# Kernel tuning notes

Hardware: AMD Instinct MI355X
Metric: run time of the kernel (lower is better)

The kernel has to match this reference:

```python
import jax, jax.numpy as jnp
import numpy as np

K = 1024          # num_embeddings
D = 128           # embedding_dim
EMA_DECAY = 0.99
EPS = 1e-5


def setup_inputs() -> dict:
    key = jax.random.key(0)
    k1, k2, k3 = jax.random.split(key, 3)
    z = jax.random.normal(k1, (64, D, 32, 32), dtype=jnp.float32)
    codebook = jax.random.normal(k2, (K, D), dtype=jnp.float32)
    ema_count = jnp.zeros((K,), dtype=jnp.float32)
    ema_weight = jax.random.normal(k3, (K, D), dtype=jnp.float32)
    return {"z": z, "codebook": codebook, "ema_count": ema_count, "ema_weight": ema_weight}


def reference(z, codebook, ema_count, ema_weight):
    B, C, H, W = z.shape
    # flatten to [N, D] in BHWC order (matches permute(0,2,3,1).view(-1, D))
    z_flat = jnp.transpose(z, (0, 2, 3, 1)).reshape(-1, D)  # [N, D]

    # squared euclidean distances [N, K]
    distances = (
        jnp.sum(z_flat * z_flat, axis=1, keepdims=True)
        + jnp.sum(codebook * codebook, axis=1)
        - 2.0 * jnp.matmul(z_flat, codebook.T)
    )
    indices = jnp.argmin(distances, axis=1)  # [N] int

    # gather instead of one-hot @ codebook (same math)
    quantized_flat = codebook[indices]  # [N, D]
    # NOTE: faithful to original: raw view of BHWC-ordered flat buffer into z.shape
    quantized = quantized_flat.reshape(z.shape)

    # EMA statistics (no_grad in original): segment sums instead of one-hot matmuls
    encodings_sum = jax.ops.segment_sum(jnp.ones_like(indices, dtype=jnp.float32), indices, num_segments=K)
    dw = jax.ops.segment_sum(z_flat, indices, num_segments=K)  # [K, D]
    new_ema_count = EMA_DECAY * ema_count + (1.0 - EMA_DECAY) * encodings_sum
    new_ema_weight = EMA_DECAY * ema_weight + (1.0 - EMA_DECAY) * dw
    n = jnp.sum(new_ema_count)
    weights = (new_ema_count + EPS) / (n + K * EPS) * n
    new_codebook = new_ema_weight / weights[:, None]

    commitment_loss = jnp.mean((jax.lax.stop_gradient(quantized) - z) ** 2)
    codebook_loss = jnp.mean((quantized - jax.lax.stop_gradient(z)) ** 2)

    # straight-through estimator
    quantized_st = z + jax.lax.stop_gradient(quantized - z)

    idx_map = indices.reshape(B, H, W)
    return (quantized_st, idx_map, commitment_loss, codebook_loss,
            new_codebook, new_ema_count, new_ema_weight)
```

## Files before the change

### kernel.cpp

```cpp
#include <hip/hip_runtime.h>

#define NVEC 65536
#define KCB  1024
#define DIM  128
#define HW   1024
#define CHUNK 64
#define NCHUNKS (NVEC / CHUNK)

typedef __bf16 b16;
typedef b16 b16x8 __attribute__((ext_vector_type(8)));
typedef float f32x16 __attribute__((ext_vector_type(16)));

static __device__ __forceinline__ unsigned short f2bf(float f) {
  unsigned int x = __float_as_uint(f);
  unsigned int r = x + 0x7fffu + ((x >> 16) & 1u);
  return (unsigned short)(r >> 16);
}

__global__ void k_prep(const float* __restrict__ cb, const float* __restrict__ emw,
                       uint4* __restrict__ cbt, float* __restrict__ ccb,
                       double* __restrict__ cc64, float* __restrict__ out6,
                       int* __restrict__ hist) {
  const int t = blockIdx.x * blockDim.x + threadIdx.x;
  const int kc = t >> 11, u = t & 2047;
  const int code7 = u & 127, dch = u >> 7;
  const float* src = cb + (kc * 128 + code7) * 128 + dch * 8;
  const float4 x = *(const float4*)src;
  const float4 y = *(const float4*)(src + 4);
  uint4 o;
  o.x = (unsigned)f2bf(x.x) | ((unsigned)f2bf(x.y) << 16);
  o.y = (unsigned)f2bf(x.z) | ((unsigned)f2bf(x.w) << 16);
  o.z = (unsigned)f2bf(y.x) | ((unsigned)f2bf(y.y) << 16);
  o.w = (unsigned)f2bf(y.z) | ((unsigned)f2bf(y.w) << 16);
  cbt[t] = o;
  const float4 e0 = *(const float4*)(emw + (size_t)t * 8);
  const float4 e1 = *(const float4*)(emw + (size_t)t * 8 + 4);
  *(float2*)(out6 + (size_t)t * 8 + 0) = make_float2(0.99f * e0.x, 0.99f * e0.y);
  *(float2*)(out6 + (size_t)t * 8 + 2) = make_float2(0.99f * e0.z, 0.99f * e0.w);
  *(float2*)(out6 + (size_t)t * 8 + 4) = make_float2(0.99f * e1.x, 0.99f * e1.y);
  *(float2*)(out6 + (size_t)t * 8 + 6) = make_float2(0.99f * e1.z, 0.99f * e1.w);
  if (t < KCB) hist[t] = 0;
  if (blockIdx.x < 4) {
    const int k = blockIdx.x * 256 + threadIdx.x;
    const float* row = cb + k * DIM;
    double s = 0.0;
#pragma unroll 8
    for (int j = 0; j < DIM; ++j) {
      const double v = (double)row[j];
      s = fma(v, v, s);
    }
    cc64[k] = s;
    ccb[k] = 512.f - 0.5f * (float)s;
  }
}

__global__ __launch_bounds__(256, 4) void k_argmin6(
    const float* __restrict__ z, const uint4* __restrict__ cbt,
    const float* __restrict__ ccb, const double* __restrict__ cc64,
    const float* __restrict__ cb, float* __restrict__ z_t,
    float* __restrict__ out1, int* __restrict__ hist) {
  __shared__ __align__(16) float zs[128][65];
  __shared__ uint2 cand[64][2];
  uint4* Bs = (uint4*)zs;
  const int tid = threadIdx.x;
  const int l = tid & 63, wv = tid >> 6;
  const int g = l >> 5;
  const int lm = l & 31;
  const int wr = (wv & 1) * 32;
  const int wc = wv >> 1;
  const int n0 = blockIdx.x * 64;
  const int b = n0 >> 10;
  const int hwbase = n0 & (HW - 1);

  {
    const int hw4 = (tid & 15) * 4;
    const int dr = tid >> 4;
    const float* src = z + (size_t)b * 131072 + hwbase + hw4;
#pragma unroll
    for (int j = 0; j < 8; ++j) {
      const int d = dr + 16 * j;
      const float4 v = *(const float4*)(src + d * 1024);
      zs[d][hw4 + 0] = v.x; zs[d][hw4 + 1] = v.y;
      zs[d][hw4 + 2] = v.z; zs[d][hw4 + 3] = v.w;
    }
  }
  __syncthreads();

#pragma unroll
  for (int jj = 0; jj < 2; ++jj) {
    const int row = (tid >> 3) + 32 * jj;
    float* dst = z_t + ((size_t)(n0 + row)) * 128;
#pragma unroll
    for (int j = 0; j < 4; ++j) {
      const int d = (j * 8 + (tid & 7)) * 4;
      float4 v;
      v.x = zs[d + 0][row]; v.y = zs[d + 1][row];
      v.z = zs[d + 2][row]; v.w = zs[d + 3][row];
      *(float4*)(dst + d) = v;
    }
  }
  uint4 afrag[8];
  {
    const int row = wr + lm;
#pragma unroll
    for (int ks = 0; ks < 8; ++ks) {
      const int d0 = ks * 16 + g * 8;
      afrag[ks].x = (unsigned)f2bf(zs[d0 + 0][row]) | ((unsigned)f2bf(zs[d0 + 1][row]) << 16);
      afrag[ks].y = (unsigned)f2bf(zs[d0 + 2][row]) | ((unsigned)f2bf(zs[d0 + 3][row]) << 16);
      afrag[ks].z = (unsigned)f2bf(zs[d0 + 4][row]) | ((unsigned)f2bf(zs[d0 + 5][row]) << 16);
      afrag[ks].w = (unsigned)f2bf(zs[d0 + 6][row]) | ((unsigned)f2bf(zs[d0 + 7][row]) << 16);
    }
  }

  unsigned pm1[16], pm2[16];
#pragma unroll
  for (int r = 0; r < 16; ++r) { pm1[r] = 0u; pm2[r] = 0u; }

  for (int kc = 0; kc < 8; ++kc) {
    __syncthreads();
#pragma unroll
    for (int i = 0; i < 8; ++i) {
      __builtin_amdgcn_global_load_lds(&cbt[kc * 2048 + wv * 512 + i * 64 + l],
                                       &Bs[wv * 512 + i * 64], 16, 0, 0);
    }
    const float cv0 = ccb[kc * 128 + (wc * 2 + 0) * 32 + lm];
    const float cv1 = ccb[kc * 128 + (wc * 2 + 1) * 32 + lm];
    __syncthreads();

    f32x16 a0, a1;
#pragma unroll
    for (int j = 0; j < 16; ++j) { a0[j] = cv0; a1[j] = cv1; }
#pragma unroll
    for (int ks = 0; ks < 8; ++ks) {
      const b16x8 av = *reinterpret_cast<const b16x8*>(&afrag[ks]);
      const b16x8 bv0 = *reinterpret_cast<const b16x8*>(&Bs[(ks * 2 + g) * 128 + (wc * 2) * 32 + lm]);
      const b16x8 bv1 = *reinterpret_cast<const b16x8*>(&Bs[(ks * 2 + g) * 128 + (wc * 2 + 1) * 32 + lm]);
      a0 = __builtin_amdgcn_mfma_f32_32x32x16_bf16(av, bv0, a0, 0, 0, 0);
      a1 = __builtin_amdgcn_mfma_f32_32x32x16_bf16(av, bv1, a1, 0, 0, 0);
    }
    const unsigned ci0 = 1023u - (unsigned)(kc * 128 + (wc * 2) * 32 + lm);
    const unsigned ci1 = ci0 - 32u;
#pragma unroll
    for (int r = 0; r < 16; ++r) {
      {
        const unsigned uu = ((__float_as_uint(a0[r]) + 0x200u) & 0xFFFFFC00u) | ci0;
        const unsigned t = pm1[r] < uu ? pm1[r] : uu;
        pm1[r] = pm1[r] > uu ? pm1[r] : uu;
        pm2[r] = pm2[r] > t ? pm2[r] : t;
      }
      {
        const unsigned uu = ((__float_as_uint(a1[r]) + 0x200u) & 0xFFFFFC00u) | ci1;
        const unsigned t = pm1[r] < uu ? pm1[r] : uu;
        pm1[r] = pm1[r] > uu ? pm1[r] : uu;
        pm2[r] = pm2[r] > t ? pm2[r] : t;
      }
    }
  }

#pragma unroll
  for (int r = 0; r < 16; ++r) {
    unsigned u1 = pm1[r], u2 = pm2[r];
#pragma unroll
    for (int m = 1; m < 32; m <<= 1) {
      const unsigned o1 = (unsigned)__shfl_xor((int)u1, m, 64);
      const unsigned o2 = (unsigned)__shfl_xor((int)u2, m, 64);
      const unsigned s = u1 < o1 ? u1 : o1;
      u1 = u1 > o1 ? u1 : o1;
      u2 = u2 > o2 ? u2 : o2;
      u2 = u2 > s ? u2 : s;
    }
    if (lm == 0) {
      const int lrow = wr + (r & 3) + 8 * (r >> 2) + 4 * g;
      cand[lrow][wc] = make_uint2(u1, u2);
    }
  }
  __syncthreads();

  int* h = (int*)zs;
#pragma unroll
  for (int j = 0; j < 4; ++j) h[tid + 256 * j] = 0;
  __syncthreads();
  {
    const int db = l & 15, c = l >> 4;
#pragma unroll 2
    for (int it = 0; it < 16; ++it) {
      const int row = wv * 16 + it;
      const uint2 cd = cand[row][c >> 1];
      const unsigned u = (c & 1) ? cd.y : cd.x;
      int k = 1023 - (int)(u & 1023u);
      const int n = n0 + row;
      const float4* zr = (const float4*)(z_t + (size_t)n * DIM) + db * 2;
      const float4* cr = (const float4*)(cb + (size_t)k * DIM) + db * 2;
      const float4 z0 = zr[0], z1 = zr[1];
      const float4 c0 = cr[0], c1 = cr[1];
      double da = 0.0, dbb = 0.0;
      da = fma((double)z0.x, (double)c0.x, da);
      da = fma((double)z0.y, (double)c0.y, da);
      da = fma((double)z0.z, (double)c0.z, da);
      da = fma((double)z0.w, (double)c0.w, da);
      dbb = fma((double)z1.x, (double)c1.x, dbb);
      dbb = fma((double)z1.y, (double)c1.y, dbb);
      dbb = fma((double)z1.z, (double)c1.z, dbb);
      dbb = fma((double)z1.w, (double)c1.w, dbb);
      double s = da + dbb;
#pragma unroll
      for (int m = 1; m < 16; m <<= 1) s += __shfl_xor(s, m, 64);
      s = fma(-2.0, s, cc64[k]);
#pragma unroll
      for (int m = 16; m < 64; m <<= 1) {
        const double os = __shfl_xor(s, m, 64);
        const int ok = __shfl_xor(k, m, 64);
        if (os < s || (os == s && ok < k)) { s = os; k = ok; }
      }
      if (l == 0) {
        out1[n] = (float)k;
        atomicAdd(&h[k], 1);
      }
    }
  }
  __syncthreads();
#pragma unroll
  for (int j = 0; j < 4; ++j) {
    const int v = h[tid + 256 * j];
    if (v) atomicAdd(&hist[tid + 256 * j], v);
  }
}

__global__ void k_scan(const int* __restrict__ hist, const float* __restrict__ emc,
                       int* __restrict__ cursor, float* __restrict__ out5,
                       float* __restrict__ ntot) {
  __shared__ int tmp[KCB];
  __shared__ float red[16];
  const int t = threadIdx.x;
  const int v = hist[t];
  tmp[t] = v;
  __syncthreads();
  for (int off = 1; off < KCB; off <<= 1) {
    int x = 0;
    if (t >= off) x = tmp[t - off];
    __syncthreads();
    if (t >= off) tmp[t] += x;
    __syncthreads();
  }
  cursor[t] = tmp[t] - v;
  float o5 = 0.99f * emc[t] + 0.01f * (float)v;
  out5[t] = o5;
#pragma unroll
  for (int m = 32; m; m >>= 1) o5 += __shfl_xor(o5, m, 64);
  if ((t & 63) == 0) red[t >> 6] = o5;
  __syncthreads();
  if (t == 0) {
    float s = 0.f;
#pragma unroll
    for (int j = 0; j < 16; ++j) s += red[j];
    *ntot = s;
  }
}

__global__ void k_scatter(const float* __restrict__ idx_f, int* __restrict__ cursor,
                          uint2* __restrict__ ok) {
  const int n = blockIdx.x * blockDim.x + threadIdx.x;
  const int k = (int)idx_f[n];
  const int pos = atomicAdd(&cursor[k], 1);
  ok[pos] = make_uint2((unsigned)n, (unsigned)k);
}

__global__ __launch_bounds__(128) void k_chunkreduce_q(
    float* zq, const float* __restrict__ cb, const uint2* __restrict__ ok,
    float* __restrict__ out6, float* __restrict__ lossp) {
  __shared__ int so[CHUNK], sk[CHUNK];
  __shared__ float red[2];
  const int t = threadIdx.x;
  const int base = blockIdx.x * CHUNK;
  if (t < CHUNK) {
    const uint2 v = ok[base + t];
    so[t] = (int)v.x; sk[t] = (int)v.y;
  }
  __syncthreads();
  int kprev = sk[0];
  float cbv = cb[kprev * 128 + t];
  float acc = 0.f, loss = 0.f;
  int i = 0;
  while (i < CHUNK) {
    if (i + 8 <= CHUNK && sk[i] == kprev && sk[i + 7] == kprev) {
      const int n0 = so[i + 0], n1 = so[i + 1], n2 = so[i + 2], n3 = so[i + 3];
      const int n4 = so[i + 4], n5 = so[i + 5], n6 = so[i + 6], n7 = so[i + 7];
      const float v0 = zq[(size_t)n0 * 128 + t];
      const float v1 = zq[(size_t)n1 * 128 + t];
      const float v2 = zq[(size_t)n2 * 128 + t];
      const float v3 = zq[(size_t)n3 * 128 + t];
      const float v4 = zq[(size_t)n4 * 128 + t];
      const float v5 = zq[(size_t)n5 * 128 + t];
      const float v6 = zq[(size_t)n6 * 128 + t];
      const float v7 = zq[(size_t)n7 * 128 + t];
      acc += ((v0 + v1) + (v2 + v3)) + ((v4 + v5) + (v6 + v7));
      float e;
      e = cbv - v0; loss = fmaf(e, e, loss);
      e = cbv - v1; loss = fmaf(e, e, loss);
      e = cbv - v2; loss = fmaf(e, e, loss);
      e = cbv - v3; loss = fmaf(e, e, loss);
      e = cbv - v4; loss = fmaf(e, e, loss);
      e = cbv - v5; loss = fmaf(e, e, loss);
      e = cbv - v6; loss = fmaf(e, e, loss);
      e = cbv - v7; loss = fmaf(e, e, loss);
      zq[(size_t)n0 * 128 + t] = cbv; zq[(size_t)n1 * 128 + t] = cbv;
      zq[(size_t)n2 * 128 + t] = cbv; zq[(size_t)n3 * 128 + t] = cbv;
      zq[(size_t)n4 * 128 + t] = cbv; zq[(size_t)n5 * 128 + t] = cbv;
      zq[(size_t)n6 * 128 + t] = cbv; zq[(size_t)n7 * 128 + t] = cbv;
      i += 8;
    } else {
      const int kk = sk[i];
      if (kk != kprev) {
        atomicAdd(&out6[kprev * 128 + t], 0.01f * acc);
        acc = 0.f; kprev = kk;
        cbv = cb[kk * 128 + t];
      }
      const int n = so[i];
      const float v = zq[(size_t)n * 128 + t];
      acc += v;
      const float e = cbv - v; loss = fmaf(e, e, loss);
      zq[(size_t)n * 128 + t] = cbv;
      ++i;
    }
  }
  atomicAdd(&out6[kprev * 128 + t], 0.01f * acc);
#pragma unroll
  for (int m = 32; m; m >>= 1) loss += __shfl_xor(loss, m, 64);
  if ((t & 63) == 0) red[t >> 6] = loss;
  __syncthreads();
  if (t == 0) lossp[blockIdx.x] = red[0] + red[1];
}

__global__ void k_final(const float* __restrict__ out5, const float* __restrict__ out6,
                        const float* __restrict__ ntot_p, const float* __restrict__ lossp,
                        float* __restrict__ out4, float* __restrict__ out2,
                        float* __restrict__ out3) {
  __shared__ float red[4];
  const int i = blockIdx.x * blockDim.x + threadIdx.x;
  const float ntot = *ntot_p;
  const int k = i >> 7;
  const float w = (out5[k] + 1e-5f) / (ntot + KCB * 1e-5f) * ntot;
  out4[i] = out6[i] / w;
  if (blockIdx.x == 511) {
    const int t = threadIdx.x;
    float s = 0.f;
#pragma unroll
    for (int j = 0; j < NCHUNKS / 256; ++j) s += lossp[t + 256 * j];
#pragma unroll
    for (int m = 32; m; m >>= 1) s += __shfl_xor(s, m, 64);
    if ((t & 63) == 0) red[t >> 6] = s;
    __syncthreads();
    if (t == 0) {
      const float lv = (red[0] + red[1] + red[2] + red[3]) * (1.f / 8388608.f);
      *out2 = lv; *out3 = lv;
    }
  }
}

extern "C" void kernel_launch(void* const* d_in, const int* in_sizes, int n_in,
                              void* d_out, int out_size, void* d_ws, size_t ws_size,
                              hipStream_t stream) {
  (void)in_sizes; (void)n_in; (void)out_size; (void)ws_size;
  const float* z   = (const float*)d_in[0];
  const float* cb  = (const float*)d_in[1];
  const float* emc = (const float*)d_in[2];
  const float* emw = (const float*)d_in[3];
  float* out = (float*)d_out;
  float* out0 = out;
  float* out1 = out + 8388608;
  float* out2 = out + 8454144;
  float* out3 = out + 8454145;
  float* out4 = out + 8454146;
  float* out5 = out + 8585218;
  float* out6 = out + 8586242;
  float* ws = (float*)d_ws;
  uint4* cbt      = (uint4*)ws;
  uint2* okbuf    = (uint2*)(ws + 65536);
  float* ccb      = ws + 327680;
  int* hist       = (int*)(ws + 328704);
  int* cursor     = (int*)(ws + 329728);
  float* ntot     = ws + 330752;
  float* lossp    = ws + 331776;
  double* cc64    = (double*)(ws + 333824);
  float* z_t = out0;

  hipLaunchKernelGGL(k_prep, dim3(64), dim3(256), 0, stream, cb, emw, cbt, ccb,
                     cc64, out6, hist);
  hipLaunchKernelGGL(k_argmin6, dim3(NVEC / 64), dim3(256), 0, stream,
                     z, cbt, ccb, cc64, cb, z_t, out1, hist);
  hipLaunchKernelGGL(k_scan, dim3(1), dim3(1024), 0, stream, hist, emc, cursor,
                     out5, ntot);
  hipLaunchKernelGGL(k_scatter, dim3(NVEC / 256), dim3(256), 0, stream, out1, cursor,
                     okbuf);
  hipLaunchKernelGGL(k_chunkreduce_q, dim3(NCHUNKS), dim3(128), 0, stream,
                     z_t, cb, okbuf, out6, lossp);
  hipLaunchKernelGGL(k_final, dim3(512), dim3(256), 0, stream, out5, out6, ntot,
                     lossp, out4, out2, out3);
}
```

Measured before the change: 128.9 us.

## Double-buffer codebook tiles in LDS and halve chunk size for reduction

```diff
diff --git a/kernel.cpp b/kernel.cpp
--- a/kernel.cpp
+++ b/kernel.cpp
@@ -4,7 +4,7 @@
 #define KCB  1024
 #define DIM  128
 #define HW   1024
-#define CHUNK 64
+#define CHUNK 32
 #define NCHUNKS (NVEC / CHUNK)
 
 typedef __bf16 b16;
@@ -54,20 +54,21 @@
   }
 }
 
-__global__ __launch_bounds__(256, 4) void k_argmin6(
+__global__ __launch_bounds__(256, 4) void k_argmin7(
     const float* __restrict__ z, const uint4* __restrict__ cbt,
     const float* __restrict__ ccb, const double* __restrict__ cc64,
     const float* __restrict__ cb, float* __restrict__ z_t,
     float* __restrict__ out1, int* __restrict__ hist) {
   __shared__ __align__(16) float zs[128][65];
   __shared__ uint2 cand[64][2];
-  uint4* Bs = (uint4*)zs;
+  uint4* Bs0 = (uint4*)zs;
+  uint4* Bs1 = ((uint4*)zs) + 1024;
   const int tid = threadIdx.x;
   const int l = tid & 63, wv = tid >> 6;
   const int g = l >> 5;
   const int lm = l & 31;
   const int wr = (wv & 1) * 32;
-  const int wc = wv >> 1;
+  const int cg = wv >> 1;
   const int n0 = blockIdx.x * 64;
   const int b = n0 >> 10;
   const int hwbase = n0 & (HW - 1);
@@ -116,44 +117,45 @@
 #pragma unroll
   for (int r = 0; r < 16; ++r) { pm1[r] = 0u; pm2[r] = 0u; }
 
-  for (int kc = 0; kc < 8; ++kc) {
+  __syncthreads();
+#pragma unroll
+  for (int i = 0; i < 4; ++i) {
+    const int dch = wv * 4 + i;
+    __builtin_amdgcn_global_load_lds(&cbt[dch * 128 + l], &Bs0[dch * 64], 16, 0, 0);
+  }
+
+  for (int c = 0; c < 16; ++c) {
     __syncthreads();
-#pragma unroll
-    for (int i = 0; i < 8; ++i) {
-      __builtin_amdgcn_global_load_lds(&cbt[kc * 2048 + wv * 512 + i * 64 + l],
-                                       &Bs[wv * 512 + i * 64], 16, 0, 0);
-    }
-    const float cv0 = ccb[kc * 128 + (wc * 2 + 0) * 32 + lm];
-    const float cv1 = ccb[kc * 128 + (wc * 2 + 1) * 32 + lm];
-    __syncthreads();
-
-    f32x16 a0, a1;
-#pragma unroll
-    for (int j = 0; j < 16; ++j) { a0[j] = cv0; a1[j] = cv1; }
+    const uint4* cur = (c & 1) ? Bs1 : Bs0;
+    uint4* nxt = (c & 1) ? Bs0 : Bs1;
+    if (c < 15) {
+      const int c1 = c + 1, kc = c1 >> 1, h = c1 & 1;
+#pragma unroll
+      for (int i = 0; i < 4; ++i) {
+        const int dch = wv * 4 + i;
+        __builtin_amdgcn_global_load_lds(&cbt[kc * 2048 + dch * 128 + h * 64 + l],
+                                         &nxt[dch * 64], 16, 0, 0);
+      }
+    }
+    const int cbase = c * 64 + cg * 32 + lm;
+    const float cv = ccb[cbase];
+    f32x16 acc;
+#pragma unroll
+    for (int j = 0; j < 16; ++j) acc[j] = cv;
 #pragma unroll
     for (int ks = 0; ks < 8; ++ks) {
       const b16x8 av = *reinterpret_cast<const b16x8*>(&afrag[ks]);
-      const b16x8 bv0 = *reinterpret_cast<const b16x8*>(&Bs[(ks * 2 + g) * 128 + (wc * 2) * 32 + lm]);
-      const b16x8 bv1 = *reinterpret_cast<const b16x8*>(&Bs[(ks * 2 + g) * 128 + (wc * 2 + 1) * 32 + lm]);
-      a0 = __builtin_amdgcn_mfma_f32_32x32x16_bf16(av, bv0, a0, 0, 0, 0);
-      a1 = __builtin_amdgcn_mfma_f32_32x32x16_bf16(av, bv1, a1, 0, 0, 0);
-    }
-    const unsigned ci0 = 1023u - (unsigned)(kc * 128 + (wc * 2) * 32 + lm);
-    const unsigned ci1 = ci0 - 32u;
+      const b16x8 bv = *reinterpret_cast<const b16x8*>(
+          &cur[(ks * 2 + g) * 64 + cg * 32 + lm]);
+      acc = __builtin_amdgcn_mfma_f32_32x32x16_bf16(av, bv, acc, 0, 0, 0);
+    }
+    const unsigned ci = 1023u - (unsigned)cbase;
 #pragma unroll
     for (int r = 0; r < 16; ++r) {
-      {
-        const unsigned uu = ((__float_as_uint(a0[r]) + 0x200u) & 0xFFFFFC00u) | ci0;
-        const unsigned t = pm1[r] < uu ? pm1[r] : uu;
-        pm1[r] = pm1[r] > uu ? pm1[r] : uu;
-        pm2[r] = pm2[r] > t ? pm2[r] : t;
-      }
-      {
-        const unsigned uu = ((__float_as_uint(a1[r]) + 0x200u) & 0xFFFFFC00u) | ci1;
-        const unsigned t = pm1[r] < uu ? pm1[r] : uu;
-        pm1[r] = pm1[r] > uu ? pm1[r] : uu;
-        pm2[r] = pm2[r] > t ? pm2[r] : t;
-      }
+      const unsigned uu = ((__float_as_uint(acc[r]) + 0x200u) & 0xFFFFFC00u) | ci;
+      const unsigned tt = pm1[r] < uu ? pm1[r] : uu;
+      pm1[r] = pm1[r] > uu ? pm1[r] : uu;
+      pm2[r] = pm2[r] > tt ? pm2[r] : tt;
     }
   }
 
@@ -171,7 +173,7 @@
     }
     if (lm == 0) {
       const int lrow = wr + (r & 3) + 8 * (r >> 2) + 4 * g;
-      cand[lrow][wc] = make_uint2(u1, u2);
+      cand[lrow][cg] = make_uint2(u1, u2);
     }
   }
   __syncthreads();
@@ -386,7 +388,7 @@
 
   hipLaunchKernelGGL(k_prep, dim3(64), dim3(256), 0, stream, cb, emw, cbt, ccb,
                      cc64, out6, hist);
-  hipLaunchKernelGGL(k_argmin6, dim3(NVEC / 64), dim3(256), 0, stream,
+  hipLaunchKernelGGL(k_argmin7, dim3(NVEC / 64), dim3(256), 0, stream,
                      z, cbt, ccb, cc64, cb, z_t, out1, hist);
   hipLaunchKernelGGL(k_scan, dim3(1), dim3(1024), 0, stream, hist, emc, cursor,
                      out5, ntot);
```

New measurement: 132.0 us. +2.4%, slower.
